# Kernel optimization log

Measured on AMD Instinct MI355X. Metric: run time of the kernel, lower is better.

## Reference

```python
import jax, jax.numpy as jnp
import numpy as np

B, C, H, W = 2, 256, 64, 64
HEADS, SR = 8, 4
D = C // HEADS          # head dim = 32
N = H * W               # query length = 4096
EPS = 1e-5


def _conv(x, w, stride=1, pad=0, groups=1, b=None):
    out = jax.lax.conv_general_dilated(
        x, w, (stride, stride), [(pad, pad), (pad, pad)],
        dimension_numbers=('NCHW', 'OIHW', 'NCHW'),
        feature_group_count=groups)
    if b is not None:
        out = out + b[None, :, None, None]
    return out


def _bn(x, p):
    # p: [4, C] = (gamma, beta, running_mean, running_var), eval-mode BN
    g, b, m, v = p[0], p[1], p[2], p[3]
    s = g / jnp.sqrt(v + EPS)
    return (x - m[None, :, None, None]) * s[None, :, None, None] + b[None, :, None, None]


def setup_inputs() -> dict:
    key = jax.random.key(0)
    ks = iter(jax.random.split(key, 32))
    nrm = lambda shape, s=0.05: jax.random.normal(next(ks), shape, jnp.float32) * s
    def bnp():
        return jnp.stack([jnp.ones((C,), jnp.float32), jnp.zeros((C,), jnp.float32),
                          jax.random.normal(next(ks), (C,), jnp.float32) * 0.1,
                          jax.random.uniform(next(ks), (C,), jnp.float32) + 0.5])
    return dict(
        x=jax.random.normal(next(ks), (B, C, H, W), jnp.float32),
        relative_pos_enc=jax.random.normal(next(ks), (B, 2, 64, 64), jnp.float32),
        q_w=nrm((C, C, 1, 1)), q_b=jnp.zeros((C,), jnp.float32),
        kv_w=nrm((2 * C, C, 1, 1)), kv_b=jnp.zeros((2 * C,), jnp.float32),
        sr1_dw_w=nrm((C, 1, SR + 3, SR + 3)), sr1_bn1=bnp(),
        sr1_pw_w=nrm((C, 1, 1, 1), 0.5), sr1_bn2=bnp(),
        sr2_dw_w=nrm((C, 1, SR // 2 + 3, SR // 2 + 3)), sr2_bn1=bnp(),
        sr2_pw_w=nrm((C, 1, 1, 1), 0.5), sr2_bn2=bnp(),
        local_w=nrm((C, 1, 3, 3)), local_b=jnp.zeros((C,), jnp.float32),
    )


def reference(x, relative_pos_enc, q_w, q_b, kv_w, kv_b,
              sr1_dw_w, sr1_bn1, sr1_pw_w, sr1_bn2,
              sr2_dw_w, sr2_bn1, sr2_pw_w, sr2_bn2,
              local_w, local_b):
    scale = D ** -0.5
    # q: 1x1 conv -> [B, heads, N, D]; both branches use the FIRST half of heads
    q = _conv(x, q_w, b=q_b).reshape(B, HEADS, D, N).transpose(0, 1, 3, 2)
    qh = q[:, :HEADS // 2]

    def branch(dw_w, bn1, pw_w, bn2, stride, pad, rpe_slice):
        # SR path: depthwise conv + BN + ReLU, depthwise 1x1 + BN
        y = jax.nn.relu(_bn(_conv(x, dw_w, stride, pad, groups=C), bn1))
        y = _bn(_conv(y, pw_w, groups=C), bn2)
        # local 3x3 depthwise mixing with residual
        y = _conv(y, local_w, pad=1, groups=C, b=local_b) + y
        kv = _conv(y, kv_w, b=kv_b)                # [B, 2C, h', w']
        k, v = jnp.split(kv, 2, axis=1)
        L = 2 * y.shape[2] * y.shape[3]            # channel-fold doubles kv length
        k = k.reshape(B, HEADS // 2, D, L)
        v = v.reshape(B, HEADS // 2, D, L).transpose(0, 1, 3, 2)
        attn = jnp.einsum('bhnd,bhdl->bhnl', qh, k) * scale
        rpe = jax.image.resize(rpe_slice, (B, 1, N, L), method='bicubic')
        attn = jax.nn.softmax(attn + rpe, axis=-1)
        return jnp.einsum('bhnl,bhld->bhnd', attn, v)

    x1 = branch(sr1_dw_w, sr1_bn1, sr1_pw_w, sr1_bn2,
                SR, (SR + 3) // 2, relative_pos_enc[:, 0:1])
    x2 = branch(sr2_dw_w, sr2_bn1, sr2_pw_w, sr2_bn2,
                SR // 2, (SR // 2 + 3) // 2, relative_pos_enc[:, 1:2])
    out = jnp.concatenate([x1, x2], axis=-1)       # [B, heads//2, N, 2D]
    return out.reshape(B, C, H, W)
```

## Files before the change

kernel.cpp:

```cpp
#include <hip/hip_runtime.h>
#include <hip/hip_bf16.h>
#include <math.h>

#define NB 2
#define NC 256
#define HWIN 4096
#define NN 4096
#define ND 32
#define NHH 4
#define EPSV 1e-5f

typedef short short8 __attribute__((ext_vector_type(8)));
typedef float f32x4 __attribute__((ext_vector_type(4)));
typedef unsigned short u16;
typedef unsigned int u32;

#define OFF_T1   0
#define OFF_T2   262144
#define OFF_Q    1310720
#define OFF_KT1  1835008
#define OFF_VT1  1900544
#define OFF_KT2  1966080
#define OFF_VT2  2228224
#define OFF_RCT1 2490368
#define OFF_RCT2 2531328
#define OFF_WT   2695168
#define OFF_PO   2826240
#define OFF_PS   4923392
#define OFF_QWT  5054464
#define OFF_LWP  5087232

#define QSCALE 0.2550437314857726f
#define LOG2E  1.4426950408889634f

__device__ __forceinline__ u16 f2bf(float x) {
  unsigned u = __float_as_uint(x);
  u += 0x7fffu + ((u >> 16) & 1u);
  return (u16)(u >> 16);
}

__device__ __forceinline__ u32 pk_bf16(float a, float b) {
  __hip_bfloat162 h = __float22bfloat162_rn(make_float2(a, b));
  u32 r; __builtin_memcpy(&r, &h, 4);
  return r;
}

__device__ __forceinline__ float keysw(float t) {
  t = fabsf(t);
  float w;
  if (t < 1.f)       w = ((1.5f*t - 2.5f)*t)*t + 1.f;
  else if (t < 2.f)  w = ((-0.5f*t + 2.5f)*t - 4.f)*t + 2.f;
  else               w = 0.f;
  return w;
}

template<int KS, int STR, int PAD, int OH>
__device__ __forceinline__ void dwconv_body(int idx, const float* __restrict__ x,
    const float* __restrict__ dww, const float* __restrict__ bn1,
    const float* __restrict__ pww, const float* __restrict__ bn2,
    float* __restrict__ tout) {
  const int hw = OH*OH;
  int s = idx % hw; int c = (idx/hw) % NC; int b = idx/(hw*NC);
  int oy = s / OH, ox = s % OH;
  const float* xp = x + (b*NC + c)*HWIN;
  const float* wp = dww + c*KS*KS;
  float acc = 0.f;
  #pragma unroll
  for (int ky = 0; ky < KS; ++ky) {
    int iy = oy*STR - PAD + ky;
    if (iy < 0 || iy >= 64) continue;
    #pragma unroll
    for (int kx = 0; kx < KS; ++kx) {
      int ix = ox*STR - PAD + kx;
      if (ix < 0 || ix >= 64) continue;
      acc += xp[iy*64 + ix] * wp[ky*KS + kx];
    }
  }
  float s1 = bn1[c] * rsqrtf(bn1[3*NC + c] + EPSV);
  float z = (acc - bn1[2*NC + c])*s1 + bn1[NC + c];
  z = fmaxf(z, 0.f);
  float s2 = bn2[c] * rsqrtf(bn2[3*NC + c] + EPSV);
  z = z * (pww[c]*s2) + (bn2[NC + c] - bn2[2*NC + c]*s2);
  tout[((size_t)(b*hw + s))*NC + c] = z;
}

__device__ __forceinline__ void rpe_body(int idx, const float* __restrict__ rpe,
                                         u16* __restrict__ rcT, int L, int ch) {
  int r = idx & 63; int l = (idx >> 6) % L; int b = idx / (64*L);
  float f = ((float)l + 0.5f)*(64.f/(float)L) - 0.5f;
  int i0 = (int)floorf(f) - 1;
  const float* rp = rpe + ((b*2 + ch)*64 + r)*64;
  float v = 0.f, wsum = 0.f;
  #pragma unroll
  for (int j = 0; j < 4; ++j) {
    int i = i0 + j;
    if (i >= 0 && i < 64) {
      float w = keysw(f - (float)i);
      v += w * rp[i]; wsum += w;
    }
  }
  rcT[((size_t)(b*L + l))*80 + 4 + r] = f2bf(v / wsum);
}

__global__ void __launch_bounds__(256) prep_kernel(
    const float* __restrict__ x,
    const float* __restrict__ dw1, const float* __restrict__ bn11,
    const float* __restrict__ pw1, const float* __restrict__ bn12, float* __restrict__ t1,
    const float* __restrict__ dw2, const float* __restrict__ bn21,
    const float* __restrict__ pw2, const float* __restrict__ bn22, float* __restrict__ t2,
    const float* __restrict__ rpe, u16* __restrict__ rct1, u16* __restrict__ rct2,
    const float* __restrict__ kvw, float* __restrict__ wtp,
    const float* __restrict__ qw, float* __restrict__ qwp2,
    const float* __restrict__ lw, float* __restrict__ lwp) {
  int blk = blockIdx.x;
  int t = threadIdx.x;
  if (blk < 512) {
    dwconv_body<7,4,3,16>(blk*256 + t, x, dw1, bn11, pw1, bn12, t1);
  } else if (blk < 2560) {
    dwconv_body<5,2,2,32>((blk-512)*256 + t, x, dw2, bn21, pw2, bn22, t2);
  } else if (blk < 2816) {
    rpe_body((blk-2560)*256 + t, rpe, rct1, 512, 0);
  } else if (blk < 3840) {
    rpe_body((blk-2816)*256 + t, rpe, rct2, 2048, 1);
  } else if (blk < 3968) {
    int idx = (blk-3840)*256 + t;
    float4 vv = *(const float4*)(kvw + (size_t)idx*4);
    int o = idx >> 6, c4 = idx & 63;
    *(float4*)(wtp + ((size_t)(c4*512 + o))*4) = vv;
  } else if (blk < 4000) {
    int idx = (blk-3968)*256 + t;
    float4 vv = *(const float4*)(qw + (size_t)idx*4);
    int oc = idx >> 6, c0 = (idx & 63)*4;
    int ocq = oc >> 2, r = oc & 3;
    qwp2[((size_t)((c0+0)*32 + ocq))*4 + r] = vv.x;
    qwp2[((size_t)((c0+1)*32 + ocq))*4 + r] = vv.y;
    qwp2[((size_t)((c0+2)*32 + ocq))*4 + r] = vv.z;
    qwp2[((size_t)((c0+3)*32 + ocq))*4 + r] = vv.w;
  } else {
    int c = t;
    #pragma unroll
    for (int tp = 0; tp < 9; ++tp) lwp[tp*256 + c] = lw[c*9 + tp];
  }
}

__global__ void __launch_bounds__(256) localkv_kernel(
    const float* __restrict__ t1T, const float* __restrict__ t2T,
    const float* __restrict__ lwp, const float* __restrict__ lb,
    const float* __restrict__ wtp, const float* __restrict__ kvb,
    u16* __restrict__ kt1, u16* __restrict__ vt1,
    u16* __restrict__ kt2, u16* __restrict__ vt2,
    const float* __restrict__ x, const float* __restrict__ qwp2,
    const float* __restrict__ qb, u16* __restrict__ q) {
  __shared__ float sbuf[NC*32];
  int blk = blockIdx.x, tid = threadIdx.x;
  if (blk < 320) {
    int kv = blk & 1, ti = blk >> 1;
    const float* tT; u16 *kT, *vT; int OH, hw, b, s0;
    if (ti < 32) { tT = t1T; kT = kt1; vT = vt1; OH = 16; hw = 256;  b = ti >> 4; s0 = (ti & 15)*16; }
    else { int v2 = ti-32; tT = t2T; kT = kt2; vT = vt2; OH = 32; hw = 1024; b = v2 >> 6; s0 = (v2 & 63)*16; }
    int oy = s0 / OH, ox0 = s0 % OH;
    const float* tb = tT + (size_t)b*hw*NC;
    int cl = tid & 63, spg = tid >> 6;
    int c0 = cl*4;
    f32x4 wt9[9];
    #pragma unroll
    for (int tp = 0; tp < 9; ++tp) wt9[tp] = *(const f32x4*)(lwp + tp*256 + c0);
    f32x4 lb4 = *(const f32x4*)(lb + c0);
    #pragma unroll
    for (int i = 0; i < 4; ++i) {
      int ox = ox0 + spg*4 + i;
      f32x4 a = lb4;
      #pragma unroll
      for (int dy = 0; dy < 3; ++dy) {
        int iy = oy + dy - 1;
        if (iy < 0 || iy >= OH) continue;
        #pragma unroll
        for (int dx = 0; dx < 3; ++dx) {
          int ix = ox + dx - 1;
          if (ix < 0 || ix >= OH) continue;
          f32x4 tv = *(const f32x4*)(tb + (size_t)(iy*OH + ix)*NC + c0);
          a += tv * wt9[dy*3 + dx];
        }
      }
      a += *(const f32x4*)(tb + (size_t)(oy*OH + ox)*NC + c0);
      *(f32x4*)(sbuf + (spg*4 + i)*NC + c0) = a;
    }
    __syncthreads();
    int ol = tid & 127, sph = tid >> 7;
    int obase = kv*256 + ol;
    float acc0[8], acc1[8];
    float b0 = kvb[obase], b1 = kvb[obase + 128];
    #pragma unroll
    for (int j = 0; j < 8; ++j) { acc0[j] = b0; acc1[j] = b1; }
    #pragma unroll 2
    for (int c4 = 0; c4 < 64; ++c4) {
      f32x4 w0 = *(const f32x4*)(wtp + ((size_t)(c4*512 + obase))*4);
      f32x4 w1 = *(const f32x4*)(wtp + ((size_t)(c4*512 + obase + 128))*4);
      #pragma unroll
      for (int j2 = 0; j2 < 8; ++j2) {
        f32x4 y4 = *(const f32x4*)(sbuf + (sph*8 + j2)*NC + c4*4);
        #pragma unroll
        for (int j = 0; j < 4; ++j) { acc0[j2] += w0[j]*y4[j]; acc1[j2] += w1[j]*y4[j]; }
      }
    }
    int L = 2*hw;
    #pragma unroll
    for (int k = 0; k < 2; ++k) {
      const float* ap = k ? acc1 : acc0;
      int o = obase + k*128;
      if (kv == 0) {
        int hh = o >> 6, e = o & 1, d = (o & 63) >> 1;
        u16* kp = kT + ((size_t)((b*NHH + hh)*L + e*hw + s0 + sph*8))*ND + d;
        #pragma unroll
        for (int j2 = 0; j2 < 8; ++j2) kp[j2*ND] = f2bf(ap[j2]);
      } else {
        int ov = o - 256;
        int hh = ov >> 6, e = ov & 1, d = (ov & 63) >> 1;
        int l0v = e*hw + s0 + sph*8;
        u16* vp = vT + ((size_t)((b*NHH + hh)*(L/64) + (l0v >> 6))*ND + d)*64 + (l0v & 63);
        #pragma unroll
        for (int j2 = 0; j2 < 8; ++j2) vp[j2] = f2bf(ap[j2]);
      }
    }
  } else {
    int qblk = blk - 320;
    int b = qblk >> 7;
    int n0 = (qblk & 127) * 32;
    const float* xb = x + (size_t)b*NC*HWIN + n0;
    #pragma unroll
    for (int j = 0; j < 8; ++j) {
      int u = tid + 256*j;
      int c = u >> 3, spq = u & 7;
      *(f32x4*)(sbuf + c*32 + spq*4) = *(const f32x4*)(xb + (size_t)c*HWIN + spq*4);
    }
    __syncthreads();
    int ocq = tid & 31, spg = tid >> 5;
    float acc[4][4];
    #pragma unroll
    for (int k = 0; k < 4; ++k) {
      float bias = qb[ocq*4 + k];
      #pragma unroll
      for (int i = 0; i < 4; ++i) acc[k][i] = bias;
    }
    #pragma unroll 4
    for (int c = 0; c < NC; ++c) {
      f32x4 w4 = *(const f32x4*)(qwp2 + ((size_t)(c*32 + ocq))*4);
      f32x4 y4 = *(const f32x4*)(sbuf + c*32 + spg*4);
      #pragma unroll
      for (int k = 0; k < 4; ++k)
        #pragma unroll
        for (int i = 0; i < 4; ++i) acc[k][i] += w4[k]*y4[i];
    }
    #pragma unroll
    for (int k = 0; k < 4; ++k) {
      int oc = ocq*4 + k;
      int h = oc >> 5, d = oc & 31;
      u16* qp = q + (((size_t)(b*NHH + h))*NN + n0 + spg*4)*ND + d;
      #pragma unroll
      for (int i = 0; i < 4; ++i) qp[i*ND] = f2bf(acc[k][i]*QSCALE);
    }
  }
}

__global__ void __launch_bounds__(256) attn_kernel(
    const u16* __restrict__ qbf,
    const u16* __restrict__ kt1, const u16* __restrict__ vt1, const u16* __restrict__ rct1,
    const u16* __restrict__ kt2, const u16* __restrict__ vt2, const u16* __restrict__ rct2,
    u32* __restrict__ po32, float* __restrict__ ps,
    float* __restrict__ out) {
  __shared__ u16 kbuf[64*32];
  __shared__ u16 vbuf[32*64];
  __shared__ u32 pbuf_all[4][16*32];
  int u = blockIdx.x;
  int br, b, hh, rb, chunk;
  if (u < 512) { br = 0; b = u >> 8; hh = (u >> 6) & 3; rb = u & 63; chunk = 0; }
  else { int v = u - 512; br = 1; chunk = v & 3; rb = (v >> 2) & 63; hh = (v >> 8) & 3; b = v >> 10; }
  int L = br ? 2048 : 512;
  const u16* kT  = br ? kt2 : kt1;
  const u16* vT  = br ? vt2 : vt1;
  const u16* rcT = br ? rct2 : rct1;
  int l0base = chunk * 512;
  int tid = threadIdx.x;
  int w = tid >> 6, lane = tid & 63;
  int g = lane >> 4, lo = lane & 15;
  u32* pbuf = pbuf_all[w];
  u16* pbuf16 = (u16*)pbuf;
  int n = rb*64 + w*16 + lo;

  const u16* kbase = kT + (size_t)(b*NHH + hh)*L*ND;
  const u16* vbase = vT + (size_t)(b*NHH + hh)*ND*L;
  const u16* rcTb  = rcT + (size_t)b*L*80;

  short8 qf = *(const short8*)(qbf + (((size_t)(b*NHH + hh))*NN + n)*ND + 8*g);

  float fr = ((float)n + 0.5f)*(1.f/64.f) - 0.5f;
  int ri0 = (int)floorf(fr) - 1;
  int a = (w < 2) ? rb - 2 : rb - 1;
  int rmin = a & ~3;
  float wr4[4]; float wsum = 0.f;
  #pragma unroll
  for (int j = 0; j < 4; ++j) {
    int i = ri0 + j;
    float wv = (i >= 0 && i < 64) ? keysw(fr - (float)i) : 0.f;
    wr4[j] = wv; wsum += wv;
  }
  float invw = LOG2E / wsum;
  float wt8[8];
  #pragma unroll
  for (int s = 0; s < 8; ++s) {
    float acc = 0.f;
    #pragma unroll
    for (int j = 0; j < 4; ++j)
      acc += (ri0 + j - rmin == s) ? wr4[j]*invw : 0.f;
    wt8[s] = acc;
  }
  short8 wtf;
  {
    u32 p0 = pk_bf16(wt8[0], wt8[1]), p1 = pk_bf16(wt8[2], wt8[3]);
    u32 p2 = pk_bf16(wt8[4], wt8[5]), p3 = pk_bf16(wt8[6], wt8[7]);
    uint4 uu = make_uint4(p0, p1, p2, p3);
    wtf = __builtin_bit_cast(short8, uu);
    if (g != 0) wtf = (short8)0;
  }
  const u16* rcrow0 = rcTb + (rmin + 4);

  const f32x4 zero = {0.f, 0.f, 0.f, 0.f};
  float ssum = 0.f;
  f32x4 o0 = zero, o1 = zero;

  int kr_row = tid >> 2, kr_col = (tid & 3)*8;
  int kr_sw  = ((kr_row >> 1) & 3)*8;
  int vr_row = tid >> 3, vr_col = (tid & 7)*8;
  int vr_sw  = (vr_row & 7)*8;
  int ksw = ((lo >> 1) & 3)*8;
  int vsw = (lo & 7)*8;
  int psw4 = (lo & 7)*4;
  int psw8 = (lo & 7)*8;

  auto stageLoad = [&](short8& kr, short8& vr, int l0) {
    kr = *(const short8*)(kbase + (size_t)(l0 + kr_row)*ND + kr_col);
    vr = *(const short8*)(vbase + (size_t)(l0 >> 6)*(ND*64) + vr_row*64 + vr_col);
  };
  auto stageStore = [&](short8 kr, short8 vr) {
    *(short8*)(kbuf + kr_row*32 + (kr_col ^ kr_sw)) = kr;
    *(short8*)(vbuf + vr_row*64 + (vr_col ^ vr_sw)) = vr;
  };
  auto loadRC = [&](uint4 (&rc)[4], int l0) {
    #pragma unroll
    for (int c = 0; c < 4; ++c) {
      const u16* arow = rcrow0 + (size_t)(l0 + 16*c + lo)*80;
      uint2 ra = *(const uint2*)arow;
      uint2 rb2 = *(const uint2*)(arow + 4);
      rc[c] = make_uint4(ra.x, ra.y, rb2.x, rb2.y);
    }
  };

  short8 kr, vr;
  uint4 rcA[4], rcB[4];
  stageLoad(kr, vr, l0base);
  loadRC(rcA, l0base);

  for (int t = 0; t < 8; ++t) {
    stageStore(kr, vr);
    __syncthreads();
    if (t < 7) { stageLoad(kr, vr, l0base + (t+1)*64); loadRC(rcB, l0base + (t+1)*64); }
    f32x4 s4[4];
    #pragma unroll
    for (int c = 0; c < 4; ++c) {
      short8 rcf = __builtin_bit_cast(short8, rcA[c]);
      f32x4 accr = __builtin_amdgcn_mfma_f32_16x16x32_bf16(rcf, wtf, zero, 0, 0, 0);
      short8 kf = *(const short8*)(kbuf + (16*c + lo)*32 + ((8*g) ^ ksw));
      s4[c] = __builtin_amdgcn_mfma_f32_16x16x32_bf16(kf, qf, accr, 0, 0, 0);
    }
    float psum = 0.f;
    u32 pk[8];
    #pragma unroll
    for (int c = 0; c < 4; ++c) {
      float p0 = __builtin_amdgcn_exp2f(s4[c][0]);
      float p1 = __builtin_amdgcn_exp2f(s4[c][1]);
      float p2 = __builtin_amdgcn_exp2f(s4[c][2]);
      float p3 = __builtin_amdgcn_exp2f(s4[c][3]);
      psum += (p0 + p1) + (p2 + p3);
      pk[2*c]   = pk_bf16(p0, p1);
      pk[2*c+1] = pk_bf16(p2, p3);
    }
    ssum += psum;
    #pragma unroll
    for (int c = 0; c < 4; ++c)
      *(uint2*)(pbuf + lo*32 + ((8*c + 2*g) ^ psw4)) = make_uint2(pk[2*c], pk[2*c+1]);
    short8 pf0 = *(const short8*)(pbuf16 + lo*64 + ((8*g) ^ psw8));
    short8 pf1 = *(const short8*)(pbuf16 + lo*64 + ((32 + 8*g) ^ psw8));
    short8 v00 = *(const short8*)(vbuf + lo*64 + ((8*g) ^ vsw));
    short8 v01 = *(const short8*)(vbuf + lo*64 + ((32 + 8*g) ^ vsw));
    short8 v10 = *(const short8*)(vbuf + (16 + lo)*64 + ((8*g) ^ vsw));
    short8 v11 = *(const short8*)(vbuf + (16 + lo)*64 + ((32 + 8*g) ^ vsw));
    o0 = __builtin_amdgcn_mfma_f32_16x16x32_bf16(v00, pf0, o0, 0, 0, 0);
    o1 = __builtin_amdgcn_mfma_f32_16x16x32_bf16(v10, pf0, o1, 0, 0, 0);
    o0 = __builtin_amdgcn_mfma_f32_16x16x32_bf16(v01, pf1, o0, 0, 0, 0);
    o1 = __builtin_amdgcn_mfma_f32_16x16x32_bf16(v11, pf1, o1, 0, 0, 0);
    if (t < 7) {
      #pragma unroll
      for (int j = 0; j < 4; ++j) rcA[j] = rcB[j];
    }
    __syncthreads();
  }

  ssum += __shfl_xor(ssum, 16, 64);
  ssum += __shfl_xor(ssum, 32, 64);
  if (br == 0) {
    float inv = 1.f/ssum;
    f32x4 w0 = o0*inv, w1 = o1*inv;
    float* op = out + ((size_t)((b*NC + hh*64 + rb)*64 + (w*16 + lo)))*64;
    *(f32x4*)(op + 4*g)      = w0;
    *(f32x4*)(op + 16 + 4*g) = w1;
  } else {
    int bh = b*NHH + hh;
    int row = bh*NN + n;
    u32* pop = po32 + ((size_t)chunk*32768 + row)*16;
    pop[2*g]     = pk_bf16(o0[0], o0[1]);
    pop[2*g + 1] = pk_bf16(o0[2], o0[3]);
    pop[8 + 2*g]     = pk_bf16(o1[0], o1[1]);
    pop[8 + 2*g + 1] = pk_bf16(o1[2], o1[3]);
    if (g == 0) ps[(size_t)chunk*32768 + row] = ssum;
  }
}

__global__ void __launch_bounds__(256) combine_kernel(
    const u32* __restrict__ po32, const float* __restrict__ ps,
    float* __restrict__ out) {
  int gid = blockIdx.x*256 + threadIdx.x;
  int row = gid >> 2, part = gid & 3;
  float sden = ps[row] + ps[32768 + row] + ps[65536 + row] + ps[98304 + row];
  float inv = 1.f/sden;
  float o[8];
  #pragma unroll
  for (int i = 0; i < 8; ++i) o[i] = 0.f;
  #pragma unroll
  for (int chunk = 0; chunk < 4; ++chunk) {
    const u32* pp = po32 + ((size_t)chunk*32768 + row)*16 + part*4;
    uint4 a = *(const uint4*)pp;
    u32 av[4] = {a.x, a.y, a.z, a.w};
    #pragma unroll
    for (int j = 0; j < 4; ++j) {
      o[2*j]   += __uint_as_float(av[j] << 16);
      o[2*j+1] += __uint_as_float(av[j] & 0xffff0000u);
    }
  }
  int bh = row >> 12, n = row & 4095;
  float* op = out + ((size_t)(((bh>>2)*NC + (bh&3)*64 + (n>>6))*64 + (n&63)))*64 + 32 + part*8;
  #pragma unroll
  for (int j = 0; j < 2; ++j) {
    f32x4 v = {o[4*j]*inv, o[4*j+1]*inv, o[4*j+2]*inv, o[4*j+3]*inv};
    *(f32x4*)(op + 4*j) = v;
  }
}

extern "C" void kernel_launch(void* const* d_in, const int* in_sizes, int n_in,
                              void* d_out, int out_size, void* d_ws, size_t ws_size,
                              hipStream_t stream) {
  const float* x    = (const float*)d_in[0];
  const float* rpe  = (const float*)d_in[1];
  const float* qw   = (const float*)d_in[2];
  const float* qb   = (const float*)d_in[3];
  const float* kvw  = (const float*)d_in[4];
  const float* kvb  = (const float*)d_in[5];
  const float* dw1  = (const float*)d_in[6];
  const float* bn11 = (const float*)d_in[7];
  const float* pw1  = (const float*)d_in[8];
  const float* bn12 = (const float*)d_in[9];
  const float* dw2  = (const float*)d_in[10];
  const float* bn21 = (const float*)d_in[11];
  const float* pw2  = (const float*)d_in[12];
  const float* bn22 = (const float*)d_in[13];
  const float* lw   = (const float*)d_in[14];
  const float* lb   = (const float*)d_in[15];
  float* out = (float*)d_out;
  float* ws  = (float*)d_ws;

  float* t1   = ws + OFF_T1;
  float* t2   = ws + OFF_T2;
  u16*   q    = (u16*)(ws + OFF_Q);
  u16*   kt1  = (u16*)(ws + OFF_KT1);
  u16*   vt1  = (u16*)(ws + OFF_VT1);
  u16*   kt2  = (u16*)(ws + OFF_KT2);
  u16*   vt2  = (u16*)(ws + OFF_VT2);
  u16*   rct1 = (u16*)(ws + OFF_RCT1);
  u16*   rct2 = (u16*)(ws + OFF_RCT2);
  float* wtp  = ws + OFF_WT;
  u32*   po32 = (u32*)(ws + OFF_PO);
  float* ps   = ws + OFF_PS;
  float* qwp2 = ws + OFF_QWT;
  float* lwp  = ws + OFF_LWP;

  hipLaunchKernelGGL(prep_kernel, dim3(4001), dim3(256), 0, stream,
                     x, dw1, bn11, pw1, bn12, t1, dw2, bn21, pw2, bn22, t2,
                     rpe, rct1, rct2, kvw, wtp, qw, qwp2, lw, lwp);
  hipLaunchKernelGGL(localkv_kernel, dim3(576), dim3(256), 0, stream,
                     t1, t2, lwp, lb, wtp, kvb, kt1, vt1, kt2, vt2, x, qwp2, qb, q);
  hipLaunchKernelGGL(attn_kernel, dim3(2560), dim3(256), 0, stream,
                     q, kt1, vt1, rct1, kt2, vt2, rct2, po32, ps, out);
  hipLaunchKernelGGL(combine_kernel, dim3(512), dim3(256), 0, stream,
                     po32, ps, out);
}
```

Baseline: 188.0 us.

## Drop split-L attention and combine kernel; halve localkv tiles and shared memory

The attention kernel no longer splits branch 2's 2048-long key axis into four chunks with a separate combine kernel. Each block now loops over the full key length and writes normalized output directly, and the long branch-2 blocks are scheduled first. This removes the partial-output and denominator writes, the bf16 rounding of partials, and one launch, at the cost of fewer and longer attention blocks (1024 instead of 2560). The localkv kernel now processes 8 spatial positions per block instead of 16 and stages the q projection input in two halves, shrinking shared memory from 32KB to 16KB and doubling the kv block count to raise occupancy.

```diff
diff --git a/kernel.cpp b/kernel.cpp
--- a/kernel.cpp
+++ b/kernel.cpp
@@ -25,8 +25,6 @@
 #define OFF_RCT1 2490368
 #define OFF_RCT2 2531328
 #define OFF_WT   2695168
-#define OFF_PO   2826240
-#define OFF_PS   4923392
 #define OFF_QWT  5054464
 #define OFF_LWP  5087232
 
@@ -151,13 +149,13 @@
     u16* __restrict__ kt2, u16* __restrict__ vt2,
     const float* __restrict__ x, const float* __restrict__ qwp2,
     const float* __restrict__ qb, u16* __restrict__ q) {
-  __shared__ float sbuf[NC*32];
+  __shared__ float sbuf[128*32];
   int blk = blockIdx.x, tid = threadIdx.x;
-  if (blk < 320) {
+  if (blk < 640) {
     int kv = blk & 1, ti = blk >> 1;
     const float* tT; u16 *kT, *vT; int OH, hw, b, s0;
-    if (ti < 32) { tT = t1T; kT = kt1; vT = vt1; OH = 16; hw = 256;  b = ti >> 4; s0 = (ti & 15)*16; }
-    else { int v2 = ti-32; tT = t2T; kT = kt2; vT = vt2; OH = 32; hw = 1024; b = v2 >> 6; s0 = (v2 & 63)*16; }
+    if (ti < 64) { tT = t1T; kT = kt1; vT = vt1; OH = 16; hw = 256;  b = ti >> 5; s0 = (ti & 31)*8; }
+    else { int v2 = ti-64; tT = t2T; kT = kt2; vT = vt2; OH = 32; hw = 1024; b = v2 >> 7; s0 = (v2 & 127)*8; }
     int oy = s0 / OH, ox0 = s0 % OH;
     const float* tb = tT + (size_t)b*hw*NC;
     int cl = tid & 63, spg = tid >> 6;
@@ -167,8 +165,9 @@
     for (int tp = 0; tp < 9; ++tp) wt9[tp] = *(const f32x4*)(lwp + tp*256 + c0);
     f32x4 lb4 = *(const f32x4*)(lb + c0);
     #pragma unroll
-    for (int i = 0; i < 4; ++i) {
-      int ox = ox0 + spg*4 + i;
+    for (int i = 0; i < 2; ++i) {
+      int sp = spg*2 + i;
+      int ox = ox0 + sp;
       f32x4 a = lb4;
       #pragma unroll
       for (int dy = 0; dy < 3; ++dy) {
@@ -183,57 +182,48 @@
         }
       }
       a += *(const f32x4*)(tb + (size_t)(oy*OH + ox)*NC + c0);
-      *(f32x4*)(sbuf + (spg*4 + i)*NC + c0) = a;
+      *(f32x4*)(sbuf + sp*NC + c0) = a;
     }
     __syncthreads();
     int ol = tid & 127, sph = tid >> 7;
-    int obase = kv*256 + ol;
-    float acc0[8], acc1[8];
-    float b0 = kvb[obase], b1 = kvb[obase + 128];
-    #pragma unroll
-    for (int j = 0; j < 8; ++j) { acc0[j] = b0; acc1[j] = b1; }
+    int o0i = kv*256 + ol, o1i = o0i + 128;
+    float acc0[4], acc1[4];
+    float b0 = kvb[o0i], b1 = kvb[o1i];
+    #pragma unroll
+    for (int i = 0; i < 4; ++i) { acc0[i] = b0; acc1[i] = b1; }
     #pragma unroll 2
     for (int c4 = 0; c4 < 64; ++c4) {
-      f32x4 w0 = *(const f32x4*)(wtp + ((size_t)(c4*512 + obase))*4);
-      f32x4 w1 = *(const f32x4*)(wtp + ((size_t)(c4*512 + obase + 128))*4);
-      #pragma unroll
-      for (int j2 = 0; j2 < 8; ++j2) {
-        f32x4 y4 = *(const f32x4*)(sbuf + (sph*8 + j2)*NC + c4*4);
+      f32x4 w0 = *(const f32x4*)(wtp + ((size_t)(c4*512 + o0i))*4);
+      f32x4 w1 = *(const f32x4*)(wtp + ((size_t)(c4*512 + o1i))*4);
+      #pragma unroll
+      for (int i = 0; i < 4; ++i) {
+        f32x4 y4 = *(const f32x4*)(sbuf + (sph*4 + i)*NC + c4*4);
         #pragma unroll
-        for (int j = 0; j < 4; ++j) { acc0[j2] += w0[j]*y4[j]; acc1[j2] += w1[j]*y4[j]; }
+        for (int j = 0; j < 4; ++j) { acc0[i] += w0[j]*y4[j]; acc1[i] += w1[j]*y4[j]; }
       }
     }
-    int L = 2*hw;
+    int L2 = 2*hw;
     #pragma unroll
     for (int k = 0; k < 2; ++k) {
       const float* ap = k ? acc1 : acc0;
-      int o = obase + k*128;
+      int oo = ol + k*128;
+      int hh = oo >> 6, r = oo & 63, d = r >> 1, e = r & 1;
       if (kv == 0) {
-        int hh = o >> 6, e = o & 1, d = (o & 63) >> 1;
-        u16* kp = kT + ((size_t)((b*NHH + hh)*L + e*hw + s0 + sph*8))*ND + d;
+        u16* kp = kT + ((size_t)((b*NHH + hh)*L2 + e*hw + s0 + sph*4))*ND + d;
         #pragma unroll
-        for (int j2 = 0; j2 < 8; ++j2) kp[j2*ND] = f2bf(ap[j2]);
+        for (int j = 0; j < 4; ++j) kp[j*ND] = f2bf(ap[j]);
       } else {
-        int ov = o - 256;
-        int hh = ov >> 6, e = ov & 1, d = (ov & 63) >> 1;
-        int l0v = e*hw + s0 + sph*8;
-        u16* vp = vT + ((size_t)((b*NHH + hh)*(L/64) + (l0v >> 6))*ND + d)*64 + (l0v & 63);
+        int l0v = e*hw + s0 + sph*4;
+        u16* vp = vT + ((size_t)((b*NHH + hh)*(L2/64) + (l0v >> 6))*ND + d)*64 + (l0v & 63);
         #pragma unroll
-        for (int j2 = 0; j2 < 8; ++j2) vp[j2] = f2bf(ap[j2]);
+        for (int j = 0; j < 4; ++j) vp[j] = f2bf(ap[j]);
       }
     }
   } else {
-    int qblk = blk - 320;
+    int qblk = blk - 640;
     int b = qblk >> 7;
     int n0 = (qblk & 127) * 32;
     const float* xb = x + (size_t)b*NC*HWIN + n0;
-    #pragma unroll
-    for (int j = 0; j < 8; ++j) {
-      int u = tid + 256*j;
-      int c = u >> 3, spq = u & 7;
-      *(f32x4*)(sbuf + c*32 + spq*4) = *(const f32x4*)(xb + (size_t)c*HWIN + spq*4);
-    }
-    __syncthreads();
     int ocq = tid & 31, spg = tid >> 5;
     float acc[4][4];
     #pragma unroll
@@ -242,14 +232,27 @@
       #pragma unroll
       for (int i = 0; i < 4; ++i) acc[k][i] = bias;
     }
-    #pragma unroll 4
-    for (int c = 0; c < NC; ++c) {
-      f32x4 w4 = *(const f32x4*)(qwp2 + ((size_t)(c*32 + ocq))*4);
-      f32x4 y4 = *(const f32x4*)(sbuf + c*32 + spg*4);
-      #pragma unroll
-      for (int k = 0; k < 4; ++k)
+    #pragma unroll
+    for (int half = 0; half < 2; ++half) {
+      #pragma unroll
+      for (int j = 0; j < 4; ++j) {
+        int u = tid + 256*j;
+        int c = u >> 3, spq = u & 7;
+        *(f32x4*)(sbuf + c*32 + spq*4) =
+            *(const f32x4*)(xb + (size_t)(half*128 + c)*HWIN + spq*4);
+      }
+      __syncthreads();
+      #pragma unroll 4
+      for (int c = 0; c < 128; ++c) {
+        int cg = half*128 + c;
+        f32x4 w4 = *(const f32x4*)(qwp2 + ((size_t)(cg*32 + ocq))*4);
+        f32x4 y4 = *(const f32x4*)(sbuf + c*32 + spg*4);
         #pragma unroll
-        for (int i = 0; i < 4; ++i) acc[k][i] += w4[k]*y4[i];
+        for (int k = 0; k < 4; ++k)
+          #pragma unroll
+          for (int i = 0; i < 4; ++i) acc[k][i] += w4[k]*y4[i];
+      }
+      __syncthreads();
     }
     #pragma unroll
     for (int k = 0; k < 4; ++k) {
@@ -266,20 +269,19 @@
     const u16* __restrict__ qbf,
     const u16* __restrict__ kt1, const u16* __restrict__ vt1, const u16* __restrict__ rct1,
     const u16* __restrict__ kt2, const u16* __restrict__ vt2, const u16* __restrict__ rct2,
-    u32* __restrict__ po32, float* __restrict__ ps,
     float* __restrict__ out) {
   __shared__ u16 kbuf[64*32];
   __shared__ u16 vbuf[32*64];
   __shared__ u32 pbuf_all[4][16*32];
   int u = blockIdx.x;
-  int br, b, hh, rb, chunk;
-  if (u < 512) { br = 0; b = u >> 8; hh = (u >> 6) & 3; rb = u & 63; chunk = 0; }
-  else { int v = u - 512; br = 1; chunk = v & 3; rb = (v >> 2) & 63; hh = (v >> 8) & 3; b = v >> 10; }
+  int br, b, hh, rb;
+  if (u < 512) { br = 1; b = u >> 8; hh = (u >> 6) & 3; rb = u & 63; }
+  else { int v = u - 512; br = 0; b = v >> 8; hh = (v >> 6) & 3; rb = v & 63; }
   int L = br ? 2048 : 512;
+  int nt = br ? 32 : 8;
   const u16* kT  = br ? kt2 : kt1;
   const u16* vT  = br ? vt2 : vt1;
   const u16* rcT = br ? rct2 : rct1;
-  int l0base = chunk * 512;
   int tid = threadIdx.x;
   int w = tid >> 6, lane = tid & 63;
   int g = lane >> 4, lo = lane & 15;
@@ -357,13 +359,13 @@
 
   short8 kr, vr;
   uint4 rcA[4], rcB[4];
-  stageLoad(kr, vr, l0base);
-  loadRC(rcA, l0base);
-
-  for (int t = 0; t < 8; ++t) {
+  stageLoad(kr, vr, 0);
+  loadRC(rcA, 0);
+
+  for (int t = 0; t < nt; ++t) {
     stageStore(kr, vr);
     __syncthreads();
-    if (t < 7) { stageLoad(kr, vr, l0base + (t+1)*64); loadRC(rcB, l0base + (t+1)*64); }
+    if (t < nt-1) { stageLoad(kr, vr, (t+1)*64); loadRC(rcB, (t+1)*64); }
     f32x4 s4[4];
     #pragma unroll
     for (int c = 0; c < 4; ++c) {
@@ -398,7 +400,7 @@
     o1 = __builtin_amdgcn_mfma_f32_16x16x32_bf16(v10, pf0, o1, 0, 0, 0);
     o0 = __builtin_amdgcn_mfma_f32_16x16x32_bf16(v01, pf1, o0, 0, 0, 0);
     o1 = __builtin_amdgcn_mfma_f32_16x16x32_bf16(v11, pf1, o1, 0, 0, 0);
-    if (t < 7) {
+    if (t < nt-1) {
       #pragma unroll
       for (int j = 0; j < 4; ++j) rcA[j] = rcB[j];
     }
@@ -407,52 +409,11 @@
 
   ssum += __shfl_xor(ssum, 16, 64);
   ssum += __shfl_xor(ssum, 32, 64);
-  if (br == 0) {
-    float inv = 1.f/ssum;
-    f32x4 w0 = o0*inv, w1 = o1*inv;
-    float* op = out + ((size_t)((b*NC + hh*64 + rb)*64 + (w*16 + lo)))*64;
-    *(f32x4*)(op + 4*g)      = w0;
-    *(f32x4*)(op + 16 + 4*g) = w1;
-  } else {
-    int bh = b*NHH + hh;
-    int row = bh*NN + n;
-    u32* pop = po32 + ((size_t)chunk*32768 + row)*16;
-    pop[2*g]     = pk_bf16(o0[0], o0[1]);
-    pop[2*g + 1] = pk_bf16(o0[2], o0[3]);
-    pop[8 + 2*g]     = pk_bf16(o1[0], o1[1]);
-    pop[8 + 2*g + 1] = pk_bf16(o1[2], o1[3]);
-    if (g == 0) ps[(size_t)chunk*32768 + row] = ssum;
-  }
-}
-
-__global__ void __launch_bounds__(256) combine_kernel(
-    const u32* __restrict__ po32, const float* __restrict__ ps,
-    float* __restrict__ out) {
-  int gid = blockIdx.x*256 + threadIdx.x;
-  int row = gid >> 2, part = gid & 3;
-  float sden = ps[row] + ps[32768 + row] + ps[65536 + row] + ps[98304 + row];
-  float inv = 1.f/sden;
-  float o[8];
-  #pragma unroll
-  for (int i = 0; i < 8; ++i) o[i] = 0.f;
-  #pragma unroll
-  for (int chunk = 0; chunk < 4; ++chunk) {
-    const u32* pp = po32 + ((size_t)chunk*32768 + row)*16 + part*4;
-    uint4 a = *(const uint4*)pp;
-    u32 av[4] = {a.x, a.y, a.z, a.w};
-    #pragma unroll
-    for (int j = 0; j < 4; ++j) {
-      o[2*j]   += __uint_as_float(av[j] << 16);
-      o[2*j+1] += __uint_as_float(av[j] & 0xffff0000u);
-    }
-  }
-  int bh = row >> 12, n = row & 4095;
-  float* op = out + ((size_t)(((bh>>2)*NC + (bh&3)*64 + (n>>6))*64 + (n&63)))*64 + 32 + part*8;
-  #pragma unroll
-  for (int j = 0; j < 2; ++j) {
-    f32x4 v = {o[4*j]*inv, o[4*j+1]*inv, o[4*j+2]*inv, o[4*j+3]*inv};
-    *(f32x4*)(op + 4*j) = v;
-  }
+  float inv = 1.f/ssum;
+  f32x4 w0 = o0*inv, w1 = o1*inv;
+  float* op = out + ((size_t)((b*NC + hh*64 + rb)*64 + (w*16 + lo)))*64 + (br ? 32 : 0);
+  *(f32x4*)(op + 4*g)      = w0;
+  *(f32x4*)(op + 16 + 4*g) = w1;
 }
 
 extern "C" void kernel_launch(void* const* d_in, const int* in_sizes, int n_in,
@@ -487,18 +448,14 @@
   u16*   rct1 = (u16*)(ws + OFF_RCT1);
   u16*   rct2 = (u16*)(ws + OFF_RCT2);
   float* wtp  = ws + OFF_WT;
-  u32*   po32 = (u32*)(ws + OFF_PO);
-  float* ps   = ws + OFF_PS;
   float* qwp2 = ws + OFF_QWT;
   float* lwp  = ws + OFF_LWP;
 
   hipLaunchKernelGGL(prep_kernel, dim3(4001), dim3(256), 0, stream,
                      x, dw1, bn11, pw1, bn12, t1, dw2, bn21, pw2, bn22, t2,
                      rpe, rct1, rct2, kvw, wtp, qw, qwp2, lw, lwp);
-  hipLaunchKernelGGL(localkv_kernel, dim3(576), dim3(256), 0, stream,
+  hipLaunchKernelGGL(localkv_kernel, dim3(896), dim3(256), 0, stream,
                      t1, t2, lwp, lb, wtp, kvb, kt1, vt1, kt2, vt2, x, qwp2, qb, q);
-  hipLaunchKernelGGL(attn_kernel, dim3(2560), dim3(256), 0, stream,
-                     q, kt1, vt1, rct1, kt2, vt2, rct2, po32, ps, out);
-  hipLaunchKernelGGL(combine_kernel, dim3(512), dim3(256), 0, stream,
-                     po32, ps, out);
-}
+  hipLaunchKernelGGL(attn_kernel, dim3(1024), dim3(256), 0, stream,
+                     q, kt1, vt1, rct1, kt2, vt2, rct2, out);
+}
```

New measurement: 171.3 us. 8.9% less time.
